# Performance work log

Hardware: AMD Instinct MI355X
Metric: run time of the kernel (lower is better)

## Reference

```python
import jax, jax.numpy as jnp
import numpy as np
import math

D_MODEL = 2048
K = 64
W = 512              # window_size
STRIDE = W // 2      # = 256
EMA_ALPHA = 0.9
N_RETRIEVE = 8
EPS = 1e-12


def _build_cheby(k, w):
    # cheby_mat[k, n] = cos(k * arccos(t_n)), t_n = cos(pi*(2n+1)/(2w))
    ns = np.arange(w, dtype=np.float64)
    t = np.cos(np.pi * (2 * ns + 1) / (2 * w))
    ks = np.arange(k, dtype=np.float64)
    return jnp.asarray(np.cos(ks[:, None] * np.arccos(t)[None, :]), dtype=jnp.float32)


def setup_inputs() -> dict:
    key = jax.random.key(0)
    ks = jax.random.split(key, 5)
    B, S = 2, 8192
    scan_out = jax.random.normal(ks[0], (B, S, D_MODEL), dtype=jnp.float32)
    buf = jax.random.normal(ks[1], (W, D_MODEL), dtype=jnp.float32)  # pre-filled circular buffer
    # unit-modulus random-phase complex roles: r_k[d] = exp(i*theta)
    phases = jax.random.uniform(ks[2], (K, D_MODEL), dtype=jnp.float32) * (2.0 * math.pi)
    roles_real = jnp.cos(phases)
    roles_imag = jnp.sin(phases)
    w_bands = 1.0 / (jnp.arange(K, dtype=jnp.float32) + 1.0)  # w_init = 1/(k+1)
    retrieve_proj_w = jax.random.normal(ks[3], (D_MODEL, D_MODEL), dtype=jnp.float32) * 0.02
    inject_gate = jnp.zeros((1,), dtype=jnp.float32)
    cheby_mat = _build_cheby(K, W)
    return dict(scan_out=scan_out, buf=buf, roles_real=roles_real, roles_imag=roles_imag,
                w_bands=w_bands, retrieve_proj_w=retrieve_proj_w, inject_gate=inject_gate,
                cheby_mat=cheby_mat)


def reference(scan_out, buf, roles_real, roles_imag, w_bands, retrieve_proj_w, inject_gate, cheby_mat):
    S = scan_out.shape[1]
    h_mean = scan_out.mean(axis=0)                      # [S, D] batch-mean like torch code
    n_chunks = S // STRIDE
    chunks = h_mean.reshape(n_chunks, STRIDE, D_MODEL)  # each chunk triggers one bind

    init = (buf, jnp.int32(0),
            jnp.zeros((K, D_MODEL), jnp.float32),   # c_past
            jnp.zeros((D_MODEL,), jnp.float32),     # V_mem_real
            jnp.zeros((D_MODEL,), jnp.float32),     # V_mem_imag
            jnp.zeros((K,), jnp.float32),           # _coeff_norms (EMA)
            jnp.zeros((K,), jnp.float32))           # spectral_delta

    def step(carry, chunk):
        b, pos, c_past, vr, vi, cnorms, _ = carry
        # circular-buffer write of `stride` tokens starting at pos
        b = jax.lax.dynamic_update_slice(b, chunk, (pos, 0))
        pos = (pos + STRIDE) % W
        order = (jnp.arange(W, dtype=jnp.int32) + pos) % W   # oldest-first reorder
        data = b[order]                                      # [W, D]
        # Chebyshev coefficients: c = (2/W) * cheby_mat @ data, c0 halved
        coeffs = (2.0 / W) * (cheby_mat @ data)              # [K, D]
        coeffs = coeffs.at[0].multiply(0.5)
        # HRR-normalized bind into holographic memory via EMA
        norms = jnp.maximum(jnp.linalg.norm(coeffs, axis=-1, keepdims=True), EPS)
        cn = coeffs / norms
        cnorms = EMA_ALPHA * cnorms + (1.0 - EMA_ALPHA) * norms[:, 0]
        vr = EMA_ALPHA * vr + (1.0 - EMA_ALPHA) * (cn * roles_real).sum(axis=0)
        vi = EMA_ALPHA * vi + (1.0 - EMA_ALPHA) * (cn * roles_imag).sum(axis=0)
        # spectral delta vs previous window's coefficients
        delta = jnp.linalg.norm(coeffs - c_past, axis=-1)    # [K]
        return (b, pos, coeffs, vr, vi, cnorms, delta), None

    (b, pos, c_now, vr, vi, cnorms, delta), _ = jax.lax.scan(step, init, chunks)

    # retrieve: unbind top-J bands by spectral delta, denormalize, weight, project
    _, top = jax.lax.top_k(delta, N_RETRIEVE)                # [J]
    rr = roles_real[top]
    ri = roles_imag[top]
    retrieved = (vr[None, :] * rr + vi[None, :] * ri) * jnp.maximum(cnorms[top], EPS)[:, None]  # [J, D]
    weights = jax.nn.softplus(w_bands[top])                  # [J]
    ctx = (weights[:, None] * retrieved).sum(axis=0)         # [D]
    out = (ctx @ retrieve_proj_w.T) * jax.nn.sigmoid(inject_gate[0])  # [D]
    return out, delta, vr, vi
```

## Files before the change

kernel.cpp:

```cpp
#include <hip/hip_runtime.h>
#include <math.h>

#define D_MODEL 2048
#define KB_ 64
#define NCHUNK 32

typedef __bf16 bf16;
typedef __attribute__((ext_vector_type(8))) __bf16 bf16x8;
typedef __attribute__((ext_vector_type(4))) __bf16 bf16x4;
typedef __attribute__((ext_vector_type(4))) float f32x4;

#define OFF_COEFFS 0
#define OFF_NSQ    (32 * 64 * 2048)
#define OFF_NORMS  (OFF_NSQ + 32 * 64 * 32)
#define OFF_VR     (OFF_NORMS + 2048)
#define OFF_VI     (OFF_VR + 2048)
#define OFF_DSQ    (OFF_VI + 2048)
#define OFF_CTX    (OFF_DSQ + 64)

__device__ __forceinline__ void load_stage(
    const float* __restrict__ scan, const float* __restrict__ buf,
    int c, int nb, int n0, int dcol, float4* ra, float4* rb)
{
  if (c == 0 && nb < 4) {
    const float* bp = buf + (256 + nb * 64 + n0) * 2048 + dcol;
#pragma unroll
    for (int i = 0; i < 4; ++i) { ra[i] = *(const float4*)(bp + i * 2048); rb[i] = ra[i]; }
  } else {
    const float* p0 = scan + (c * 256 - 256 + nb * 64 + n0) * 2048 + dcol;
    const float* p1 = p0 + 8192 * 2048;
#pragma unroll
    for (int i = 0; i < 4; ++i) {
      ra[i] = *(const float4*)(p0 + i * 2048);
      rb[i] = *(const float4*)(p1 + i * 2048);
    }
  }
}

__device__ __forceinline__ void store_stage(
    bf16* Bsbuf, int n0, int d4, const float4* ra, const float4* rb)
{
  float4 m0 = make_float4(0.5f * (ra[0].x + rb[0].x), 0.5f * (ra[0].y + rb[0].y),
                          0.5f * (ra[0].z + rb[0].z), 0.5f * (ra[0].w + rb[0].w));
  float4 m1 = make_float4(0.5f * (ra[1].x + rb[1].x), 0.5f * (ra[1].y + rb[1].y),
                          0.5f * (ra[1].z + rb[1].z), 0.5f * (ra[1].w + rb[1].w));
  float4 m2 = make_float4(0.5f * (ra[2].x + rb[2].x), 0.5f * (ra[2].y + rb[2].y),
                          0.5f * (ra[2].z + rb[2].z), 0.5f * (ra[2].w + rb[2].w));
  float4 m3 = make_float4(0.5f * (ra[3].x + rb[3].x), 0.5f * (ra[3].y + rb[3].y),
                          0.5f * (ra[3].z + rb[3].z), 0.5f * (ra[3].w + rb[3].w));
  bf16x4 e0 = {(bf16)m0.x, (bf16)m1.x, (bf16)m2.x, (bf16)m3.x};
  bf16x4 e1 = {(bf16)m0.y, (bf16)m1.y, (bf16)m2.y, (bf16)m3.y};
  bf16x4 e2 = {(bf16)m0.z, (bf16)m1.z, (bf16)m2.z, (bf16)m3.z};
  bf16x4 e3 = {(bf16)m0.w, (bf16)m1.w, (bf16)m2.w, (bf16)m3.w};
  *(bf16x4*)(Bsbuf + (d4 + 0) * 72 + n0) = e0;
  *(bf16x4*)(Bsbuf + (d4 + 1) * 72 + n0) = e1;
  *(bf16x4*)(Bsbuf + (d4 + 2) * 72 + n0) = e2;
  *(bf16x4*)(Bsbuf + (d4 + 3) * 72 + n0) = e3;
}

__global__ __launch_bounds__(256, 4) void k1_fused(
    const float* __restrict__ scan, const float* __restrict__ buf,
    const float* __restrict__ cheby, float* __restrict__ coeffs,
    float* __restrict__ nsq, float* __restrict__ vzero)
{
  __shared__ bf16 Bs[2][64 * 72];

  const int t = threadIdx.x;
  const int dt = blockIdx.x;
  const int c  = blockIdx.y;
  const int w = t >> 6, lane = t & 63;
  const int quad = lane >> 4, r16 = lane & 15;
  const int d0 = dt * 64;
  const int n0 = (t >> 4) * 4;
  const int d4 = (t & 15) * 4;
  const int dcol = d0 + d4;

  if (dt == 0 && c == 0) {
    for (int i = t; i < 4160; i += 256) vzero[i] = 0.f;
  }

  f32x4 acc[4];
#pragma unroll
  for (int tn = 0; tn < 4; ++tn) acc[tn] = (f32x4){0.f, 0.f, 0.f, 0.f};

  float4 ra[4], rb[4];
  load_stage(scan, buf, c, 0, n0, dcol, ra, rb);
  store_stage(Bs[0], n0, d4, ra, rb);
  __syncthreads();

  for (int nb = 0; nb < 8; ++nb) {
    if (nb < 7) load_stage(scan, buf, c, nb + 1, n0, dcol, ra, rb);

    const float* ab = cheby + (w * 16 + r16) * 512 + nb * 64 + quad * 8;
    float4 f0 = *(const float4*)(ab);
    float4 f1 = *(const float4*)(ab + 4);
    float4 f2 = *(const float4*)(ab + 32);
    float4 f3 = *(const float4*)(ab + 36);
    bf16x8 a0 = {(bf16)f0.x, (bf16)f0.y, (bf16)f0.z, (bf16)f0.w,
                 (bf16)f1.x, (bf16)f1.y, (bf16)f1.z, (bf16)f1.w};
    bf16x8 a1 = {(bf16)f2.x, (bf16)f2.y, (bf16)f2.z, (bf16)f2.w,
                 (bf16)f3.x, (bf16)f3.y, (bf16)f3.z, (bf16)f3.w};

    const bf16* bsr = Bs[nb & 1];
#pragma unroll
    for (int ks = 0; ks < 2; ++ks) {
      bf16x8 a = ks ? a1 : a0;
#pragma unroll
      for (int tn = 0; tn < 4; ++tn) {
        bf16x8 bfr = *(const bf16x8*)(bsr + (tn * 16 + r16) * 72 + ks * 32 + quad * 8);
        acc[tn] = __builtin_amdgcn_mfma_f32_16x16x32_bf16(a, bfr, acc[tn], 0, 0, 0);
      }
    }

    if (nb < 7) store_stage(Bs[(nb + 1) & 1], n0, d4, ra, rb);
    __syncthreads();
  }

  const float scale = 2.0f / 512.0f;
  float sq[4] = {0.f, 0.f, 0.f, 0.f};
#pragma unroll
  for (int tn = 0; tn < 4; ++tn) {
#pragma unroll
    for (int rq = 0; rq < 4; ++rq) {
      int band = w * 16 + quad * 4 + rq;
      float sc = (band == 0) ? scale * 0.5f : scale;
      float v = acc[tn][rq] * sc;
      coeffs[(c * 64 + band) * 2048 + d0 + tn * 16 + r16] = v;
      sq[rq] += v * v;
    }
  }
#pragma unroll
  for (int off = 8; off > 0; off >>= 1) {
#pragma unroll
    for (int rq = 0; rq < 4; ++rq) sq[rq] += __shfl_down(sq[rq], off);
  }
  if (r16 == 0) {
#pragma unroll
    for (int rq = 0; rq < 4; ++rq)
      nsq[(c * 64 + w * 16 + quad * 4 + rq) * 32 + dt] = sq[rq];
  }
}

__global__ __launch_bounds__(256) void k2_bind(
    const float* __restrict__ coeffs, const float* __restrict__ nsq,
    const float* __restrict__ rr, const float* __restrict__ ri,
    float* __restrict__ vr, float* __restrict__ vi,
    float* __restrict__ dsq, float* __restrict__ norms)
{
  __shared__ float inv_s[16];
  const int t = threadIdx.x, lane = t & 63;
  const int xi = blockIdx.x >> 2, kg = blockIdx.x & 3;
  const int c = blockIdx.y;
  if (t < 16) {
    int k = kg * 16 + t;
    float s = 0.f;
#pragma unroll
    for (int dtile = 0; dtile < 32; ++dtile) s += nsq[(c * 64 + k) * 32 + dtile];
    float nrm = fmaxf(sqrtf(s), 1e-12f);
    inv_s[t] = 1.0f / nrm;
    if (xi == 0) norms[c * 64 + k] = nrm;
  }
  __syncthreads();
  const int d = xi * 256 + t;
  const float wc = 0.1f * powf(0.9f, (float)(31 - c));
  float ar = 0.f, ai = 0.f;
  if (c == 31) {
    for (int kk = 0; kk < 16; ++kk) {
      int k = kg * 16 + kk;
      float cf = coeffs[(31 * 64 + k) * 2048 + d];
      float cn = cf * inv_s[kk];
      ar += cn * rr[k * 2048 + d];
      ai += cn * ri[k * 2048 + d];
      float diff = cf - coeffs[(30 * 64 + k) * 2048 + d];
      float sqv = diff * diff;
#pragma unroll
      for (int o = 32; o > 0; o >>= 1) sqv += __shfl_down(sqv, o, 64);
      if (lane == 0) atomicAdd(&dsq[k], sqv);
    }
  } else {
    for (int kk = 0; kk < 16; ++kk) {
      int k = kg * 16 + kk;
      float cn = coeffs[(c * 64 + k) * 2048 + d] * inv_s[kk];
      ar += cn * rr[k * 2048 + d];
      ai += cn * ri[k * 2048 + d];
    }
  }
  atomicAdd(&vr[d], wc * ar);
  atomicAdd(&vi[d], wc * ai);
}

__global__ __launch_bounds__(256) void k3_ctx(
    const float* __restrict__ norms, const float* __restrict__ vr,
    const float* __restrict__ vi, const float* __restrict__ rr,
    const float* __restrict__ ri, const float* __restrict__ wb,
    const float* __restrict__ dsq, float* __restrict__ dout,
    float* __restrict__ ctx)
{
  __shared__ float cn_s[64];
  __shared__ int top_s[8];
  __shared__ float wgt_s[8];
  const int t = threadIdx.x;
  const int d = blockIdx.x * 256 + t;
  if (t < 64) {
    float s = 0.f;
    for (int c = 0; c < NCHUNK; ++c) s = 0.9f * s + 0.1f * norms[c * 64 + t];
    cn_s[t] = fmaxf(s, 1e-12f);
    if (blockIdx.x == 0) dout[D_MODEL + t] = sqrtf(dsq[t]);
  }
  if (t == 0) {
    unsigned long long taken = 0ULL;
    for (int jj = 0; jj < 8; ++jj) {
      float best = -1.f;
      int bi = 0;
      for (int k = 0; k < 64; ++k) {
        float dv = dsq[k];
        if (!((taken >> k) & 1ULL) && dv > best) { best = dv; bi = k; }
      }
      taken |= (1ULL << bi);
      top_s[jj] = bi;
      wgt_s[jj] = log1pf(expf(wb[bi]));
    }
  }
  __syncthreads();
  float sr = vr[d], si = vi[d];
  dout[D_MODEL + KB_ + d] = sr;
  dout[D_MODEL + KB_ + D_MODEL + d] = si;
  float cx = 0.f;
#pragma unroll
  for (int jj = 0; jj < 8; ++jj) {
    int k = top_s[jj];
    cx += wgt_s[jj] * (sr * rr[k * D_MODEL + d] + si * ri[k * D_MODEL + d]) * cn_s[k];
  }
  ctx[d] = cx;
}

__global__ __launch_bounds__(256) void k4_gemv(
    const float* __restrict__ Wp, const float* __restrict__ ctx,
    const float* __restrict__ gate, float* __restrict__ dout)
{
  const int tid = threadIdx.x;
  const int lane = tid & 63;
  const int w = tid >> 6;
  const int row = blockIdx.x * 4 + w;
  const float* p = Wp + row * D_MODEL;
  float s = 0.f;
#pragma unroll
  for (int i = 0; i < 8; ++i) {
    int e = lane * 4 + i * 256;
    float4 wv = *(const float4*)(p + e);
    float4 cv = *(const float4*)(ctx + e);
    s += wv.x * cv.x + wv.y * cv.y + wv.z * cv.z + wv.w * cv.w;
  }
#pragma unroll
  for (int o = 32; o > 0; o >>= 1) s += __shfl_down(s, o, 64);
  if (lane == 0) {
    float sig = 1.f / (1.f + expf(-gate[0]));
    dout[row] = s * sig;
  }
}

extern "C" void kernel_launch(void* const* d_in, const int* in_sizes, int n_in,
                              void* d_out, int out_size, void* d_ws, size_t ws_size,
                              hipStream_t stream) {
  const float* scan  = (const float*)d_in[0];
  const float* buf   = (const float*)d_in[1];
  const float* rr    = (const float*)d_in[2];
  const float* ri    = (const float*)d_in[3];
  const float* wb    = (const float*)d_in[4];
  const float* Wp    = (const float*)d_in[5];
  const float* gate  = (const float*)d_in[6];
  const float* cheby = (const float*)d_in[7];
  float* out = (float*)d_out;
  float* ws = (float*)d_ws;

  float* coeffs = ws + OFF_COEFFS;
  float* nsq    = ws + OFF_NSQ;
  float* norms  = ws + OFF_NORMS;
  float* vr     = ws + OFF_VR;
  float* vi     = ws + OFF_VI;
  float* dsq    = ws + OFF_DSQ;
  float* ctx    = ws + OFF_CTX;

  k1_fused<<<dim3(32, 32), 256, 0, stream>>>(scan, buf, cheby, coeffs, nsq, vr);
  k2_bind<<<dim3(32, 32), 256, 0, stream>>>(coeffs, nsq, rr, ri, vr, vi, dsq, norms);
  k3_ctx<<<8, 256, 0, stream>>>(norms, vr, vi, rr, ri, wb, dsq, out, ctx);
  k4_gemv<<<512, 256, 0, stream>>>(Wp, ctx, gate, out);
}
```

Before: 271.6 us.

## Split window projection into half-window partials to avoid rereading overlapping tokens

Each block now processes one 256-token half-window and multiplies it by both halves of the Chebyshev matrix. It writes first-half and second-half partial coefficients to separate buffers, so each overlapping token is loaded from global memory once instead of twice. The bind kernel sums the two partial buffers and recomputes per-band norms itself instead of reading precomputed partial sums. This trades extra workspace traffic (an additional coefficient buffer written and read twice) for halving the large input reads.

```diff
diff --git a/kernel.cpp b/kernel.cpp
--- a/kernel.cpp
+++ b/kernel.cpp
@@ -10,9 +10,9 @@
 typedef __attribute__((ext_vector_type(4))) __bf16 bf16x4;
 typedef __attribute__((ext_vector_type(4))) float f32x4;
 
-#define OFF_COEFFS 0
-#define OFF_NSQ    (32 * 64 * 2048)
-#define OFF_NORMS  (OFF_NSQ + 32 * 64 * 32)
+#define OFF_S      0
+#define OFF_F      (32 * 64 * 2048)
+#define OFF_NORMS  (2 * 32 * 64 * 2048)
 #define OFF_VR     (OFF_NORMS + 2048)
 #define OFF_VI     (OFF_VR + 2048)
 #define OFF_DSQ    (OFF_VI + 2048)
@@ -20,14 +20,14 @@
 
 __device__ __forceinline__ void load_stage(
     const float* __restrict__ scan, const float* __restrict__ buf,
-    int c, int nb, int n0, int dcol, float4* ra, float4* rb)
-{
-  if (c == 0 && nb < 4) {
+    int j, int nb, int n0, int dcol, float4* ra, float4* rb)
+{
+  if (j == 32) {
     const float* bp = buf + (256 + nb * 64 + n0) * 2048 + dcol;
 #pragma unroll
     for (int i = 0; i < 4; ++i) { ra[i] = *(const float4*)(bp + i * 2048); rb[i] = ra[i]; }
   } else {
-    const float* p0 = scan + (c * 256 - 256 + nb * 64 + n0) * 2048 + dcol;
+    const float* p0 = scan + (j * 256 + nb * 64 + n0) * 2048 + dcol;
     const float* p1 = p0 + 8192 * 2048;
 #pragma unroll
     for (int i = 0; i < 4; ++i) {
@@ -58,16 +58,16 @@
   *(bf16x4*)(Bsbuf + (d4 + 3) * 72 + n0) = e3;
 }
 
-__global__ __launch_bounds__(256, 4) void k1_fused(
+__global__ __launch_bounds__(256, 4) void k1_part(
     const float* __restrict__ scan, const float* __restrict__ buf,
-    const float* __restrict__ cheby, float* __restrict__ coeffs,
-    float* __restrict__ nsq, float* __restrict__ vzero)
+    const float* __restrict__ cheby, float* __restrict__ bufS,
+    float* __restrict__ bufF, float* __restrict__ vzero)
 {
   __shared__ bf16 Bs[2][64 * 72];
 
   const int t = threadIdx.x;
   const int dt = blockIdx.x;
-  const int c  = blockIdx.y;
+  const int j  = blockIdx.y;
   const int w = t >> 6, lane = t & 63;
   const int quad = lane >> 4, r16 = lane & 15;
   const int d0 = dt * 64;
@@ -75,112 +75,140 @@
   const int d4 = (t & 15) * 4;
   const int dcol = d0 + d4;
 
-  if (dt == 0 && c == 0) {
+  if (dt == 0 && j == 0) {
     for (int i = t; i < 4160; i += 256) vzero[i] = 0.f;
   }
 
-  f32x4 acc[4];
-#pragma unroll
-  for (int tn = 0; tn < 4; ++tn) acc[tn] = (f32x4){0.f, 0.f, 0.f, 0.f};
+  f32x4 accS[4], accF[4];
+#pragma unroll
+  for (int tn = 0; tn < 4; ++tn) {
+    accS[tn] = (f32x4){0.f, 0.f, 0.f, 0.f};
+    accF[tn] = (f32x4){0.f, 0.f, 0.f, 0.f};
+  }
 
   float4 ra[4], rb[4];
-  load_stage(scan, buf, c, 0, n0, dcol, ra, rb);
+  load_stage(scan, buf, j, 0, n0, dcol, ra, rb);
   store_stage(Bs[0], n0, d4, ra, rb);
   __syncthreads();
 
-  for (int nb = 0; nb < 8; ++nb) {
-    if (nb < 7) load_stage(scan, buf, c, nb + 1, n0, dcol, ra, rb);
+  for (int nb = 0; nb < 4; ++nb) {
+    if (nb < 3) load_stage(scan, buf, j, nb + 1, n0, dcol, ra, rb);
 
     const float* ab = cheby + (w * 16 + r16) * 512 + nb * 64 + quad * 8;
     float4 f0 = *(const float4*)(ab);
     float4 f1 = *(const float4*)(ab + 4);
     float4 f2 = *(const float4*)(ab + 32);
     float4 f3 = *(const float4*)(ab + 36);
-    bf16x8 a0 = {(bf16)f0.x, (bf16)f0.y, (bf16)f0.z, (bf16)f0.w,
-                 (bf16)f1.x, (bf16)f1.y, (bf16)f1.z, (bf16)f1.w};
-    bf16x8 a1 = {(bf16)f2.x, (bf16)f2.y, (bf16)f2.z, (bf16)f2.w,
-                 (bf16)f3.x, (bf16)f3.y, (bf16)f3.z, (bf16)f3.w};
+    float4 g0 = *(const float4*)(ab + 256);
+    float4 g1 = *(const float4*)(ab + 260);
+    float4 g2 = *(const float4*)(ab + 288);
+    float4 g3 = *(const float4*)(ab + 292);
+    bf16x8 aF[2] = {{(bf16)f0.x, (bf16)f0.y, (bf16)f0.z, (bf16)f0.w,
+                     (bf16)f1.x, (bf16)f1.y, (bf16)f1.z, (bf16)f1.w},
+                    {(bf16)f2.x, (bf16)f2.y, (bf16)f2.z, (bf16)f2.w,
+                     (bf16)f3.x, (bf16)f3.y, (bf16)f3.z, (bf16)f3.w}};
+    bf16x8 aS[2] = {{(bf16)g0.x, (bf16)g0.y, (bf16)g0.z, (bf16)g0.w,
+                     (bf16)g1.x, (bf16)g1.y, (bf16)g1.z, (bf16)g1.w},
+                    {(bf16)g2.x, (bf16)g2.y, (bf16)g2.z, (bf16)g2.w,
+                     (bf16)g3.x, (bf16)g3.y, (bf16)g3.z, (bf16)g3.w}};
 
     const bf16* bsr = Bs[nb & 1];
 #pragma unroll
     for (int ks = 0; ks < 2; ++ks) {
-      bf16x8 a = ks ? a1 : a0;
 #pragma unroll
       for (int tn = 0; tn < 4; ++tn) {
         bf16x8 bfr = *(const bf16x8*)(bsr + (tn * 16 + r16) * 72 + ks * 32 + quad * 8);
-        acc[tn] = __builtin_amdgcn_mfma_f32_16x16x32_bf16(a, bfr, acc[tn], 0, 0, 0);
+        accS[tn] = __builtin_amdgcn_mfma_f32_16x16x32_bf16(aS[ks], bfr, accS[tn], 0, 0, 0);
+        accF[tn] = __builtin_amdgcn_mfma_f32_16x16x32_bf16(aF[ks], bfr, accF[tn], 0, 0, 0);
       }
     }
 
-    if (nb < 7) store_stage(Bs[(nb + 1) & 1], n0, d4, ra, rb);
+    if (nb < 3) store_stage(Bs[(nb + 1) & 1], n0, d4, ra, rb);
     __syncthreads();
   }
 
   const float scale = 2.0f / 512.0f;
-  float sq[4] = {0.f, 0.f, 0.f, 0.f};
+  const int jF = (j == 32) ? 0 : j + 1;
 #pragma unroll
   for (int tn = 0; tn < 4; ++tn) {
 #pragma unroll
     for (int rq = 0; rq < 4; ++rq) {
       int band = w * 16 + quad * 4 + rq;
       float sc = (band == 0) ? scale * 0.5f : scale;
-      float v = acc[tn][rq] * sc;
-      coeffs[(c * 64 + band) * 2048 + d0 + tn * 16 + r16] = v;
-      sq[rq] += v * v;
-    }
-  }
-#pragma unroll
-  for (int off = 8; off > 0; off >>= 1) {
-#pragma unroll
-    for (int rq = 0; rq < 4; ++rq) sq[rq] += __shfl_down(sq[rq], off);
-  }
-  if (r16 == 0) {
-#pragma unroll
-    for (int rq = 0; rq < 4; ++rq)
-      nsq[(c * 64 + w * 16 + quad * 4 + rq) * 32 + dt] = sq[rq];
+      int dd = d0 + tn * 16 + r16;
+      if (j < 32) bufS[(j * 64 + band) * 2048 + dd] = accS[tn][rq] * sc;
+      if (j != 31) bufF[(jF * 64 + band) * 2048 + dd] = accF[tn][rq] * sc;
+    }
   }
 }
 
 __global__ __launch_bounds__(256) void k2_bind(
-    const float* __restrict__ coeffs, const float* __restrict__ nsq,
+    const float* __restrict__ bufS, const float* __restrict__ bufF,
     const float* __restrict__ rr, const float* __restrict__ ri,
     float* __restrict__ vr, float* __restrict__ vi,
     float* __restrict__ dsq, float* __restrict__ norms)
 {
+  __shared__ float red[4][16];
   __shared__ float inv_s[16];
-  const int t = threadIdx.x, lane = t & 63;
+  const int t = threadIdx.x, lane = t & 63, wv = t >> 6;
   const int xi = blockIdx.x >> 2, kg = blockIdx.x & 3;
   const int c = blockIdx.y;
+
+  float sq16[16];
+#pragma unroll
+  for (int kk = 0; kk < 16; ++kk) {
+    int k = kg * 16 + kk;
+    const float* ps = bufS + (c * 64 + k) * 2048 + t * 8;
+    const float* pf = bufF + (c * 64 + k) * 2048 + t * 8;
+    float4 s0 = *(const float4*)(ps);
+    float4 s1 = *(const float4*)(ps + 4);
+    float4 f0 = *(const float4*)(pf);
+    float4 f1 = *(const float4*)(pf + 4);
+    float a0 = s0.x + f0.x, a1 = s0.y + f0.y, a2 = s0.z + f0.z, a3 = s0.w + f0.w;
+    float a4 = s1.x + f1.x, a5 = s1.y + f1.y, a6 = s1.z + f1.z, a7 = s1.w + f1.w;
+    float s = a0 * a0 + a1 * a1 + a2 * a2 + a3 * a3 +
+              a4 * a4 + a5 * a5 + a6 * a6 + a7 * a7;
+#pragma unroll
+    for (int o = 32; o > 0; o >>= 1) s += __shfl_down(s, o, 64);
+    sq16[kk] = s;
+  }
+  if (lane == 0) {
+#pragma unroll
+    for (int kk = 0; kk < 16; ++kk) red[wv][kk] = sq16[kk];
+  }
+  __syncthreads();
   if (t < 16) {
-    int k = kg * 16 + t;
-    float s = 0.f;
-#pragma unroll
-    for (int dtile = 0; dtile < 32; ++dtile) s += nsq[(c * 64 + k) * 32 + dtile];
+    float s = red[0][t] + red[1][t] + red[2][t] + red[3][t];
     float nrm = fmaxf(sqrtf(s), 1e-12f);
     inv_s[t] = 1.0f / nrm;
-    if (xi == 0) norms[c * 64 + k] = nrm;
+    if (xi == 0) norms[c * 64 + kg * 16 + t] = nrm;
   }
   __syncthreads();
+
   const int d = xi * 256 + t;
   const float wc = 0.1f * powf(0.9f, (float)(31 - c));
   float ar = 0.f, ai = 0.f;
   if (c == 31) {
+#pragma unroll 4
     for (int kk = 0; kk < 16; ++kk) {
       int k = kg * 16 + kk;
-      float cf = coeffs[(31 * 64 + k) * 2048 + d];
+      float cf = bufS[(31 * 64 + k) * 2048 + d] + bufF[(31 * 64 + k) * 2048 + d];
       float cn = cf * inv_s[kk];
       ar += cn * rr[k * 2048 + d];
       ai += cn * ri[k * 2048 + d];
-      float diff = cf - coeffs[(30 * 64 + k) * 2048 + d];
+      float cp = bufS[(30 * 64 + k) * 2048 + d] + bufF[(30 * 64 + k) * 2048 + d];
+      float diff = cf - cp;
       float sqv = diff * diff;
 #pragma unroll
       for (int o = 32; o > 0; o >>= 1) sqv += __shfl_down(sqv, o, 64);
       if (lane == 0) atomicAdd(&dsq[k], sqv);
     }
   } else {
+#pragma unroll 4
     for (int kk = 0; kk < 16; ++kk) {
       int k = kg * 16 + kk;
-      float cn = coeffs[(c * 64 + k) * 2048 + d] * inv_s[kk];
+      float cf = bufS[(c * 64 + k) * 2048 + d] + bufF[(c * 64 + k) * 2048 + d];
+      float cn = cf * inv_s[kk];
       ar += cn * rr[k * 2048 + d];
       ai += cn * ri[k * 2048 + d];
     }
@@ -273,16 +301,16 @@
   float* out = (float*)d_out;
   float* ws = (float*)d_ws;
 
-  float* coeffs = ws + OFF_COEFFS;
-  float* nsq    = ws + OFF_NSQ;
-  float* norms  = ws + OFF_NORMS;
-  float* vr     = ws + OFF_VR;
-  float* vi     = ws + OFF_VI;
-  float* dsq    = ws + OFF_DSQ;
-  float* ctx    = ws + OFF_CTX;
-
-  k1_fused<<<dim3(32, 32), 256, 0, stream>>>(scan, buf, cheby, coeffs, nsq, vr);
-  k2_bind<<<dim3(32, 32), 256, 0, stream>>>(coeffs, nsq, rr, ri, vr, vi, dsq, norms);
+  float* bufS  = ws + OFF_S;
+  float* bufF  = ws + OFF_F;
+  float* norms = ws + OFF_NORMS;
+  float* vr    = ws + OFF_VR;
+  float* vi    = ws + OFF_VI;
+  float* dsq   = ws + OFF_DSQ;
+  float* ctx   = ws + OFF_CTX;
+
+  k1_part<<<dim3(32, 33), 256, 0, stream>>>(scan, buf, cheby, bufS, bufF, vr);
+  k2_bind<<<dim3(32, 32), 256, 0, stream>>>(bufS, bufF, rr, ri, vr, vi, dsq, norms);
   k3_ctx<<<8, 256, 0, stream>>>(norms, vr, vi, rr, ri, wb, dsq, out, ctx);
   k4_gemv<<<512, 256, 0, stream>>>(Wp, ctx, gate, out);
 }
```

Measured after the change: 283.7 us. 1.04x slower.

## Fuse bind into projection kernel via last-block counter; fold ctx into GEMV

Applied to the files above, without the earlier changes.

The separate bind kernel is removed. Inside k1, the last block to finish each chunk, found through an atomic counter and threadfence, computes norms and accumulates the EMA-weighted vr/vi over all 64 bands. Spectral delta moves to a small dedicated kernel, and the ctx computation is merged into the GEMV so each block rebuilds ctx in shared memory. This cuts launches and global round trips, but the bind work now runs on only 32 tail blocks, each serial over 64 bands, and every GEMV block redoes the ctx and top-k work.

```diff
diff --git a/kernel.cpp b/kernel.cpp
--- a/kernel.cpp
+++ b/kernel.cpp
@@ -16,7 +16,8 @@
 #define OFF_VR     (OFF_NORMS + 2048)
 #define OFF_VI     (OFF_VR + 2048)
 #define OFF_DSQ    (OFF_VI + 2048)
-#define OFF_CTX    (OFF_DSQ + 64)
+#define OFF_CNT    (OFF_DSQ + 64)
+#define ZERO_FLOATS (2048 + 2048 + 64 + 32)
 
 __device__ __forceinline__ void load_stage(
     const float* __restrict__ scan, const float* __restrict__ buf,
@@ -60,10 +61,14 @@
 
 __global__ __launch_bounds__(256, 4) void k1_fused(
     const float* __restrict__ scan, const float* __restrict__ buf,
-    const float* __restrict__ cheby, float* __restrict__ coeffs,
-    float* __restrict__ nsq, float* __restrict__ vzero)
+    const float* __restrict__ cheby, const float* __restrict__ rr,
+    const float* __restrict__ ri, float* __restrict__ coeffs,
+    float* __restrict__ nsq, float* __restrict__ norms,
+    float* __restrict__ vr, float* __restrict__ vi, int* __restrict__ cnt)
 {
   __shared__ bf16 Bs[2][64 * 72];
+  __shared__ float inv_s[64];
+  __shared__ int isLast;
 
   const int t = threadIdx.x;
   const int dt = blockIdx.x;
@@ -75,10 +80,6 @@
   const int d4 = (t & 15) * 4;
   const int dcol = d0 + d4;
 
-  if (dt == 0 && c == 0) {
-    for (int i = t; i < 4160; i += 256) vzero[i] = 0.f;
-  }
-
   f32x4 acc[4];
 #pragma unroll
   for (int tn = 0; tn < 4; ++tn) acc[tn] = (f32x4){0.f, 0.f, 0.f, 0.f};
@@ -139,75 +140,107 @@
     for (int rq = 0; rq < 4; ++rq)
       nsq[(c * 64 + w * 16 + quad * 4 + rq) * 32 + dt] = sq[rq];
   }
-}
-
-__global__ __launch_bounds__(256) void k2_bind(
-    const float* __restrict__ coeffs, const float* __restrict__ nsq,
-    const float* __restrict__ rr, const float* __restrict__ ri,
-    float* __restrict__ vr, float* __restrict__ vi,
-    float* __restrict__ dsq, float* __restrict__ norms)
-{
-  __shared__ float inv_s[16];
-  const int t = threadIdx.x, lane = t & 63;
-  const int xi = blockIdx.x >> 2, kg = blockIdx.x & 3;
-  const int c = blockIdx.y;
-  if (t < 16) {
-    int k = kg * 16 + t;
+
+  __threadfence();
+  if (t == 0) isLast = (atomicAdd(&cnt[c], 1) == 31);
+  __syncthreads();
+  if (!isLast) return;
+  __threadfence();
+
+  if (t < 64) {
     float s = 0.f;
 #pragma unroll
-    for (int dtile = 0; dtile < 32; ++dtile) s += nsq[(c * 64 + k) * 32 + dtile];
+    for (int dtile = 0; dtile < 32; ++dtile) s += nsq[(c * 64 + t) * 32 + dtile];
     float nrm = fmaxf(sqrtf(s), 1e-12f);
     inv_s[t] = 1.0f / nrm;
-    if (xi == 0) norms[c * 64 + k] = nrm;
-  }
-  __syncthreads();
-  const int d = xi * 256 + t;
+    norms[c * 64 + t] = nrm;
+  }
+  __syncthreads();
+
+  const int d8 = t * 8;
   const float wc = 0.1f * powf(0.9f, (float)(31 - c));
-  float ar = 0.f, ai = 0.f;
-  if (c == 31) {
-    for (int kk = 0; kk < 16; ++kk) {
-      int k = kg * 16 + kk;
-      float cf = coeffs[(31 * 64 + k) * 2048 + d];
-      float cn = cf * inv_s[kk];
-      ar += cn * rr[k * 2048 + d];
-      ai += cn * ri[k * 2048 + d];
-      float diff = cf - coeffs[(30 * 64 + k) * 2048 + d];
-      float sqv = diff * diff;
-#pragma unroll
-      for (int o = 32; o > 0; o >>= 1) sqv += __shfl_down(sqv, o, 64);
-      if (lane == 0) atomicAdd(&dsq[k], sqv);
-    }
-  } else {
-    for (int kk = 0; kk < 16; ++kk) {
-      int k = kg * 16 + kk;
-      float cn = coeffs[(c * 64 + k) * 2048 + d] * inv_s[kk];
-      ar += cn * rr[k * 2048 + d];
-      ai += cn * ri[k * 2048 + d];
-    }
-  }
-  atomicAdd(&vr[d], wc * ar);
-  atomicAdd(&vi[d], wc * ai);
-}
-
-__global__ __launch_bounds__(256) void k3_ctx(
-    const float* __restrict__ norms, const float* __restrict__ vr,
-    const float* __restrict__ vi, const float* __restrict__ rr,
-    const float* __restrict__ ri, const float* __restrict__ wb,
-    const float* __restrict__ dsq, float* __restrict__ dout,
-    float* __restrict__ ctx)
-{
+  float arx[8] = {0,0,0,0,0,0,0,0}, aix[8] = {0,0,0,0,0,0,0,0};
+#pragma unroll 4
+  for (int k = 0; k < KB_; ++k) {
+    float inv = inv_s[k];
+    const float* cp = coeffs + (c * 64 + k) * 2048 + d8;
+    const float* rp = rr + k * 2048 + d8;
+    const float* ip = ri + k * 2048 + d8;
+    float4 c0 = *(const float4*)(cp),     c1 = *(const float4*)(cp + 4);
+    float4 r0 = *(const float4*)(rp),     r1 = *(const float4*)(rp + 4);
+    float4 i0 = *(const float4*)(ip),     i1 = *(const float4*)(ip + 4);
+    arx[0] += c0.x * inv * r0.x; arx[1] += c0.y * inv * r0.y;
+    arx[2] += c0.z * inv * r0.z; arx[3] += c0.w * inv * r0.w;
+    arx[4] += c1.x * inv * r1.x; arx[5] += c1.y * inv * r1.y;
+    arx[6] += c1.z * inv * r1.z; arx[7] += c1.w * inv * r1.w;
+    aix[0] += c0.x * inv * i0.x; aix[1] += c0.y * inv * i0.y;
+    aix[2] += c0.z * inv * i0.z; aix[3] += c0.w * inv * i0.w;
+    aix[4] += c1.x * inv * i1.x; aix[5] += c1.y * inv * i1.y;
+    aix[6] += c1.z * inv * i1.z; aix[7] += c1.w * inv * i1.w;
+  }
+#pragma unroll
+  for (int i = 0; i < 8; ++i) {
+    atomicAdd(&vr[d8 + i], wc * arx[i]);
+    atomicAdd(&vi[d8 + i], wc * aix[i]);
+  }
+}
+
+__global__ __launch_bounds__(256) void kd_delta(
+    const float* __restrict__ coeffs, const float* __restrict__ vr,
+    const float* __restrict__ vi, float* __restrict__ dsq,
+    float* __restrict__ dout)
+{
+  const int blk = blockIdx.x, tid = threadIdx.x;
+  if (blk >= 64) {
+    const int d = (blk - 64) * 256 + tid;
+    dout[D_MODEL + KB_ + d] = vr[d];
+    dout[D_MODEL + KB_ + D_MODEL + d] = vi[d];
+    return;
+  }
+  const int k = blk;
+  const float* p1 = coeffs + (31 * 64 + k) * 2048;
+  const float* p0 = coeffs + (30 * 64 + k) * 2048;
+  float s = 0.f;
+#pragma unroll
+  for (int i = 0; i < 2; ++i) {
+    float4 a = *(const float4*)(p1 + tid * 4 + i * 1024);
+    float4 b = *(const float4*)(p0 + tid * 4 + i * 1024);
+    float x = a.x - b.x, y = a.y - b.y, z = a.z - b.z, ww = a.w - b.w;
+    s += x * x + y * y + z * z + ww * ww;
+  }
+#pragma unroll
+  for (int o = 32; o > 0; o >>= 1) s += __shfl_down(s, o, 64);
+  __shared__ float red[4];
+  if ((tid & 63) == 0) red[tid >> 6] = s;
+  __syncthreads();
+  if (tid == 0) {
+    float tot = red[0] + red[1] + red[2] + red[3];
+    dsq[k] = tot;
+    dout[D_MODEL + k] = sqrtf(tot);
+  }
+}
+
+__global__ __launch_bounds__(256) void k4_gemv(
+    const float* __restrict__ Wp, const float* __restrict__ norms,
+    const float* __restrict__ dsq, const float* __restrict__ wb,
+    const float* __restrict__ vr, const float* __restrict__ vi,
+    const float* __restrict__ rr, const float* __restrict__ ri,
+    const float* __restrict__ gate, float* __restrict__ dout)
+{
+  __shared__ float ctx_s[2048];
   __shared__ float cn_s[64];
   __shared__ int top_s[8];
   __shared__ float wgt_s[8];
-  const int t = threadIdx.x;
-  const int d = blockIdx.x * 256 + t;
-  if (t < 64) {
+  const int tid = threadIdx.x;
+  const int lane = tid & 63;
+  const int w = tid >> 6;
+
+  if (tid < 64) {
     float s = 0.f;
-    for (int c = 0; c < NCHUNK; ++c) s = 0.9f * s + 0.1f * norms[c * 64 + t];
-    cn_s[t] = fmaxf(s, 1e-12f);
-    if (blockIdx.x == 0) dout[D_MODEL + t] = sqrtf(dsq[t]);
-  }
-  if (t == 0) {
+    for (int c = 0; c < NCHUNK; ++c) s = 0.9f * s + 0.1f * norms[c * 64 + tid];
+    cn_s[tid] = fmaxf(s, 1e-12f);
+  }
+  if (tid == 0) {
     unsigned long long taken = 0ULL;
     for (int jj = 0; jj < 8; ++jj) {
       float best = -1.f;
@@ -222,25 +255,31 @@
     }
   }
   __syncthreads();
-  float sr = vr[d], si = vi[d];
-  dout[D_MODEL + KB_ + d] = sr;
-  dout[D_MODEL + KB_ + D_MODEL + d] = si;
-  float cx = 0.f;
-#pragma unroll
-  for (int jj = 0; jj < 8; ++jj) {
-    int k = top_s[jj];
-    cx += wgt_s[jj] * (sr * rr[k * D_MODEL + d] + si * ri[k * D_MODEL + d]) * cn_s[k];
-  }
-  ctx[d] = cx;
-}
-
-__global__ __launch_bounds__(256) void k4_gemv(
-    const float* __restrict__ Wp, const float* __restrict__ ctx,
-    const float* __restrict__ gate, float* __restrict__ dout)
-{
-  const int tid = threadIdx.x;
-  const int lane = tid & 63;
-  const int w = tid >> 6;
+
+  {
+    const int d8 = tid * 8;
+#pragma unroll
+    for (int h = 0; h < 2; ++h) {
+      const int d = d8 + h * 4;
+      float4 v_r = *(const float4*)(vr + d);
+      float4 v_i = *(const float4*)(vi + d);
+      float4 cx = make_float4(0.f, 0.f, 0.f, 0.f);
+#pragma unroll
+      for (int jj = 0; jj < 8; ++jj) {
+        int k = top_s[jj];
+        float g = wgt_s[jj] * cn_s[k];
+        float4 r = *(const float4*)(rr + k * D_MODEL + d);
+        float4 im = *(const float4*)(ri + k * D_MODEL + d);
+        cx.x += g * (v_r.x * r.x + v_i.x * im.x);
+        cx.y += g * (v_r.y * r.y + v_i.y * im.y);
+        cx.z += g * (v_r.z * r.z + v_i.z * im.z);
+        cx.w += g * (v_r.w * r.w + v_i.w * im.w);
+      }
+      *(float4*)(ctx_s + d) = cx;
+    }
+  }
+  __syncthreads();
+
   const int row = blockIdx.x * 4 + w;
   const float* p = Wp + row * D_MODEL;
   float s = 0.f;
@@ -248,7 +287,7 @@
   for (int i = 0; i < 8; ++i) {
     int e = lane * 4 + i * 256;
     float4 wv = *(const float4*)(p + e);
-    float4 cv = *(const float4*)(ctx + e);
+    float4 cv = *(const float4*)(ctx_s + e);
     s += wv.x * cv.x + wv.y * cv.y + wv.z * cv.z + wv.w * cv.w;
   }
 #pragma unroll
@@ -279,10 +318,12 @@
   float* vr     = ws + OFF_VR;
   float* vi     = ws + OFF_VI;
   float* dsq    = ws + OFF_DSQ;
-  float* ctx    = ws + OFF_CTX;
-
-  k1_fused<<<dim3(32, 32), 256, 0, stream>>>(scan, buf, cheby, coeffs, nsq, vr);
-  k2_bind<<<dim3(32, 32), 256, 0, stream>>>(coeffs, nsq, rr, ri, vr, vi, dsq, norms);
-  k3_ctx<<<8, 256, 0, stream>>>(norms, vr, vi, rr, ri, wb, dsq, out, ctx);
-  k4_gemv<<<512, 256, 0, stream>>>(Wp, ctx, gate, out);
-}
+  int*   cnt    = (int*)(ws + OFF_CNT);
+
+  hipMemsetAsync((void*)vr, 0, ZERO_FLOATS * sizeof(float), stream);
+
+  k1_fused<<<dim3(32, 32), 256, 0, stream>>>(scan, buf, cheby, rr, ri,
+                                             coeffs, nsq, norms, vr, vi, cnt);
+  kd_delta<<<72, 256, 0, stream>>>(coeffs, vr, vi, dsq, out);
+  k4_gemv<<<512, 256, 0, stream>>>(Wp, norms, dsq, wb, vr, vi, rr, ri, gate, out);
+}
```

New measurement: 485.2 us. 78.6% more time.
